# Kernel tuning notes

Measured on AMD Instinct MI355X. Metric: run time of the kernel, lower is better.

Reference implementation:

```python
import jax, jax.numpy as jnp
import numpy as np

N = 50000      # nodes
E = 600000     # edges
DIN = 128
H1, H2, H3 = 128, 128, 64
EPS = 1e-5


def setup_inputs() -> dict:
    key = jax.random.key(0)
    ks = jax.random.split(key, 12)
    x = jax.random.normal(ks[0], (N, DIN), jnp.float32)
    edge_index = jax.random.randint(ks[1], (2, E), 0, N, dtype=jnp.int32).astype(jnp.int64)
    s = lambda f: np.float32(1.0 / np.sqrt(f))
    W1 = jax.random.normal(ks[2], (DIN, H1), jnp.float32) * s(DIN)
    b1 = jnp.zeros((H1,), jnp.float32)
    W2 = jax.random.normal(ks[3], (H1, H2), jnp.float32) * s(H1)
    b2 = jnp.zeros((H2,), jnp.float32)
    W3 = jax.random.normal(ks[4], (H2, H3), jnp.float32) * s(H2)
    b3 = jnp.zeros((H3,), jnp.float32)
    g1 = 1.0 + 0.1 * jax.random.normal(ks[5], (H1,), jnp.float32)
    be1 = 0.1 * jax.random.normal(ks[6], (H1,), jnp.float32)
    g2 = 1.0 + 0.1 * jax.random.normal(ks[7], (H2,), jnp.float32)
    be2 = 0.1 * jax.random.normal(ks[8], (H2,), jnp.float32)
    return {"x": x, "edge_index": edge_index, "W1": W1, "b1": b1, "g1": g1,
            "be1": be1, "W2": W2, "b2": b2, "g2": g2, "be2": be2,
            "W3": W3, "b3": b3}


def _gcn(h_in, W, b, src_sl, dst_sl, norm, n):
    # GCNConv: h = X W; out_i = sum_{j->i} norm_ij * h_j + b  (self-loops included)
    h = h_in @ W
    msg = h[src_sl] * norm[:, None]          # [E+N, F] gather + scale
    out = jax.ops.segment_sum(msg, dst_sl, num_segments=n)
    return out + b


def _bn(x, g, b):
    # training-mode BatchNorm1d over nodes (biased variance, eps=1e-5)
    m = x.mean(0)
    v = x.var(0)
    return g * (x - m) * jax.lax.rsqrt(v + EPS) + b


def reference(x, edge_index, W1, b1, g1, be1, W2, b2, g2, be2, W3, b3):
    src, dst = edge_index[0], edge_index[1]
    loops = jnp.arange(N, dtype=src.dtype)
    src_sl = jnp.concatenate([src, loops])
    dst_sl = jnp.concatenate([dst, loops])
    deg = jax.ops.segment_sum(jnp.ones_like(dst_sl, jnp.float32), dst_sl,
                              num_segments=N)
    dinv = jnp.where(deg > 0, jax.lax.rsqrt(deg), 0.0)
    norm = dinv[src_sl] * dinv[dst_sl]       # symmetric D^-1/2 (A+I) D^-1/2

    h = _gcn(x, W1, b1, src_sl, dst_sl, norm, N)
    h = jax.nn.relu(_bn(h, g1, be1))         # dropout is identity in eval mode
    h = _gcn(h, W2, b2, src_sl, dst_sl, norm, N)
    h = jax.nn.relu(_bn(h, g2, be2))
    out = _gcn(h, W3, b3, src_sl, dst_sl, norm, N)  # [N, 64]
    return out
```

## Files before the change

### kernel.cpp

```cpp
#include <hip/hip_runtime.h>
#include <hip/hip_bf16.h>


typedef __attribute__((ext_vector_type(8))) short short8;
typedef __attribute__((ext_vector_type(4))) float f32x4;

__device__ inline unsigned short f2bf(float f) {
    unsigned int u = __float_as_uint(f);
    return (unsigned short)((u + 0x7fff + ((u >> 16) & 1)) >> 16);
}
__device__ inline float bf2f_lo(unsigned int p) { return __uint_as_float(p << 16); }
__device__ inline float bf2f_hi(unsigned int p) { return __uint_as_float(p & 0xffff0000u); }

__device__ inline void bf4_acc(uint2 v, float* a) {
    a[0] += bf2f_lo(v.x); a[1] += bf2f_hi(v.x);
    a[2] += bf2f_lo(v.y); a[3] += bf2f_hi(v.y);
}

__global__ void count_deg_kernel(const int* __restrict__ dst, int E,
                                 int* __restrict__ rowptr1) {
    int e = blockIdx.x * blockDim.x + threadIdx.x;
    if (e < E) atomicAdd(rowptr1 + dst[e], 1);
}

__global__ void dinv_deg_kernel(const int* __restrict__ rowptr, int n,
                                float* __restrict__ dinv, int* __restrict__ deg) {
    int i = blockIdx.x * blockDim.x + threadIdx.x;
    if (i < n) {
        int d = rowptr[i + 1];
        dinv[i] = rsqrtf((float)(d + 1));
        deg[i] = min(d, 63);
    }
}

__global__ void bhist_kernel(const int* __restrict__ deg, int n,
                             int* __restrict__ bh, int B) {
    __shared__ int lh[64];
    const int t = threadIdx.x;
    const int b = blockIdx.x;
    if (t < 64) lh[t] = 0;
    __syncthreads();
    const int lim = min((b + 1) * 2048, n);
    for (int i = b * 2048 + t; i < lim; i += 256) atomicAdd(&lh[deg[i]], 1);
    __syncthreads();
    if (t < 64) bh[t * B + b] = lh[t];
}

__global__ void bscan_kernel(int* __restrict__ bh, int total) {
    __shared__ int sh[256];
    const int t = threadIdx.x;
    int base = 0;
    for (int start = 0; start < total; start += 256) {
        int i = start + t;
        int v = (i < total) ? bh[i] : 0;
        sh[t] = v;
        __syncthreads();
#pragma unroll
        for (int off = 1; off < 256; off <<= 1) {
            int add = (t >= off) ? sh[t - off] : 0;
            __syncthreads();
            sh[t] += add;
            __syncthreads();
        }
        int excl = (t > 0 ? sh[t - 1] : 0) + base;
        if (i < total) bh[i] = excl;
        base += sh[255];
        __syncthreads();
    }
}

__global__ void place2_kernel(const int* __restrict__ deg, int n,
                              const int* __restrict__ bh, int B,
                              int* __restrict__ perm) {
    __shared__ int lbase[64];
    __shared__ int lcur[64];
    const int t = threadIdx.x;
    const int b = blockIdx.x;
    if (t < 64) {
        lbase[t] = bh[t * B + b];
        lcur[t] = 0;
    }
    __syncthreads();
    const int lim = min((b + 1) * 2048, n);
    for (int i = b * 2048 + t; i < lim; i += 256) {
        int d = deg[i];
        int r = atomicAdd(&lcur[d], 1);
        perm[lbase[d] + r] = i;
    }
}

__global__ __launch_bounds__(256) void scanA_kernel(int* __restrict__ data,
                                                    int total,
                                                    int* __restrict__ bsum) {
    __shared__ int sh[256];
    const int t = threadIdx.x;
    const int base = blockIdx.x * 2048 + t * 8;
    int v[8];
    int run = 0;
#pragma unroll
    for (int j = 0; j < 8; ++j) {
        int idx = base + j;
        int x = (idx < total) ? data[idx] : 0;
        run += x;
        v[j] = run;
    }
    sh[t] = run;
    __syncthreads();
#pragma unroll
    for (int off = 1; off < 256; off <<= 1) {
        int add = (t >= off) ? sh[t - off] : 0;
        __syncthreads();
        sh[t] += add;
        __syncthreads();
    }
    int prev = (t > 0) ? sh[t - 1] : 0;
#pragma unroll
    for (int j = 0; j < 8; ++j) {
        int idx = base + j;
        if (idx < total) data[idx] = v[j] + prev;
    }
    if (t == 255) bsum[blockIdx.x] = sh[255];
}

__global__ void scanB_kernel(int* __restrict__ bsum, int nb) {
    __shared__ int sh[64];
    const int t = threadIdx.x;
    sh[t] = (t < nb) ? bsum[t] : 0;
    __syncthreads();
#pragma unroll
    for (int off = 1; off < 64; off <<= 1) {
        int add = (t >= off) ? sh[t - off] : 0;
        __syncthreads();
        sh[t] += add;
        __syncthreads();
    }
    if (t < nb) bsum[t] = sh[t];
}

__global__ __launch_bounds__(256) void scanC_kernel(int* __restrict__ data,
                                                    int total,
                                                    const int* __restrict__ bsum) {
    if (blockIdx.x == 0) return;
    const int off = bsum[blockIdx.x - 1];
    const int base = blockIdx.x * 2048 + threadIdx.x * 8;
#pragma unroll
    for (int j = 0; j < 8; ++j) {
        int idx = base + j;
        if (idx < total) data[idx] += off;
    }
}

__global__ void csr_build_kernel(const int* __restrict__ src,
                                 const int* __restrict__ dst, int E,
                                 int* __restrict__ rowptr,
                                 int* __restrict__ csr_src) {
    int e = blockIdx.x * blockDim.x + threadIdx.x;
    if (e < E) {
        int pos = atomicAdd(rowptr + dst[e], 1);
        csr_src[pos] = src[e];
    }
}

__global__ void wt_bf16_kernel(const float* __restrict__ W, int NC,
                               unsigned short* __restrict__ Wt) {
    int idx = blockIdx.x * blockDim.x + threadIdx.x;
    if (idx < 128 * NC) {
        int k = idx / NC, nn = idx % NC;
        Wt[nn * 128 + k] = f2bf(W[idx]);
    }
}

__global__ void xcvt_kernel(const float* __restrict__ x,
                            unsigned short* __restrict__ xb, int total4) {
    int i = blockIdx.x * blockDim.x + threadIdx.x;
    if (i < total4) {
        float4 v = reinterpret_cast<const float4*>(x)[i];
        uint2 p;
        p.x = f2bf(v.x) | ((unsigned)f2bf(v.y) << 16);
        p.y = f2bf(v.z) | ((unsigned)f2bf(v.w) << 16);
        reinterpret_cast<uint2*>(xb)[i] = p;
    }
}

template <int NC, bool BN>
__global__ __launch_bounds__(256) void gemm_mfma(
    const unsigned short* __restrict__ A, const unsigned short* __restrict__ Wt,
    unsigned short* __restrict__ C, int n, const float* __restrict__ ss,
    const float* __restrict__ dinv) {
    __shared__ unsigned short Asd[64][136];
    __shared__ unsigned short Bsd[NC][136];
    const int tid = threadIdx.x;
    const int wave = tid >> 6;
    const int lane = tid & 63;
    const int row0 = blockIdx.x * 64;

    for (int idx = tid; idx < NC * 16; idx += 256) {
        int r = idx >> 4;
        int c = (idx & 15) * 8;
        uint4 v = *reinterpret_cast<const uint4*>(Wt + r * 128 + c);
        *reinterpret_cast<uint4*>(&Bsd[r][c]) = v;
    }
    for (int idx = tid; idx < 64 * 16; idx += 256) {
        int r = idx >> 4;
        int c = (idx & 15) * 8;
        int grow = row0 + r;
        uint4 v = make_uint4(0u, 0u, 0u, 0u);
        if (grow < n)
            v = *reinterpret_cast<const uint4*>(A + (size_t)grow * 128 + c);
        if (BN) {
            unsigned int p[4] = {v.x, v.y, v.z, v.w};
#pragma unroll
            for (int h = 0; h < 4; ++h) {
                int f = c + h * 2;
                float lo = fmaxf(fmaf(bf2f_lo(p[h]), ss[f], ss[128 + f]), 0.f);
                float hi = fmaxf(fmaf(bf2f_hi(p[h]), ss[f + 1], ss[129 + f]), 0.f);
                p[h] = f2bf(lo) | ((unsigned)f2bf(hi) << 16);
            }
            v = make_uint4(p[0], p[1], p[2], p[3]);
        }
        *reinterpret_cast<uint4*>(&Asd[r][c]) = v;
    }
    __syncthreads();

    f32x4 acc[NC / 16];
#pragma unroll
    for (int t = 0; t < NC / 16; ++t) acc[t] = (f32x4)(0.f);

    const int l15 = lane & 15;
    const int quad = lane >> 4;
#pragma unroll
    for (int kb = 0; kb < 128; kb += 32) {
        short8 a = *reinterpret_cast<const short8*>(&Asd[wave * 16 + l15][kb + quad * 8]);
#pragma unroll
        for (int t = 0; t < NC / 16; ++t) {
            short8 b = *reinterpret_cast<const short8*>(&Bsd[t * 16 + l15][kb + quad * 8]);
            acc[t] = __builtin_amdgcn_mfma_f32_16x16x32_bf16(a, b, acc[t], 0, 0, 0);
        }
    }

    const int rbase = row0 + wave * 16 + quad * 4;
    float dv[4] = {0.f, 0.f, 0.f, 0.f};
    if (rbase < n) {
        float4 d4 = *reinterpret_cast<const float4*>(dinv + rbase);
        dv[0] = d4.x; dv[1] = d4.y; dv[2] = d4.z; dv[3] = d4.w;
    }
#pragma unroll
    for (int t = 0; t < NC / 16; ++t) {
        int col = t * 16 + l15;
#pragma unroll
        for (int r = 0; r < 4; ++r) {
            int row = rbase + r;
            if (row < n)
                C[(size_t)row * NC + col] = f2bf(acc[t][r] * dv[r]);
        }
    }
}

template <int F, bool STATS, bool OBF>
__global__ __launch_bounds__(256) void aggregate_kernel(
    const unsigned short* __restrict__ hs, const int* __restrict__ csr_src,
    const int* __restrict__ rowptr, const int* __restrict__ perm,
    const float* __restrict__ dinv, const float* __restrict__ bias,
    void* __restrict__ outp, int n, float* __restrict__ stats) {
    const int LANES = F / 4;
    const int GROUPS = 256 / LANES;
    const int lane = threadIdx.x % LANES;
    const int grp = threadIdx.x / LANES;
    const int fq = lane * 4;
    const float4 b4 = *reinterpret_cast<const float4*>(bias + fq);
    float s[4] = {}, sq[4] = {};

    const int stride = gridDim.x * GROUPS * 4;

    for (int j0 = (blockIdx.x * GROUPS + grp) * 4; j0 < n; j0 += stride) {
        const int nv = min(4, n - j0);
        int nd[4], e[4], end[4];
        float acc[4][4] = {};
#pragma unroll
        for (int q = 0; q < 4; ++q) {
            if (q < nv) {
                int node = perm[j0 + q];
                nd[q] = node;
                e[q] = (node == 0) ? 0 : rowptr[node - 1];
                end[q] = rowptr[node];
            } else {
                nd[q] = -1; e[q] = 0; end[q] = 0;
            }
        }
#pragma unroll
        for (int q = 0; q < 4; ++q)
            if (nd[q] >= 0)
                bf4_acc(*reinterpret_cast<const uint2*>(hs + (size_t)nd[q] * F + fq), acc[q]);
        int rem = end[0] - e[0];
#pragma unroll
        for (int q = 1; q < 4; ++q)
            if (q < nv) rem = min(rem, end[q] - e[q]);
        for (; rem >= 2; rem -= 2) {
            int i0[4], i1[4];
#pragma unroll
            for (int q = 0; q < 4; ++q) {
                i0[q] = csr_src[e[q]];
                i1[q] = csr_src[e[q] + 1];
                e[q] += 2;
            }
            uint2 v0[4], v1[4];
#pragma unroll
            for (int q = 0; q < 4; ++q) {
                v0[q] = *reinterpret_cast<const uint2*>(hs + (size_t)i0[q] * F + fq);
                v1[q] = *reinterpret_cast<const uint2*>(hs + (size_t)i1[q] * F + fq);
            }
#pragma unroll
            for (int q = 0; q < 4; ++q) {
                bf4_acc(v0[q], acc[q]);
                bf4_acc(v1[q], acc[q]);
            }
        }
#pragma unroll
        for (int q = 0; q < 4; ++q) {
            for (; e[q] < end[q]; ++e[q]) {
                int s0 = csr_src[e[q]];
                bf4_acc(*reinterpret_cast<const uint2*>(hs + (size_t)s0 * F + fq), acc[q]);
            }
        }
#pragma unroll
        for (int q = 0; q < 4; ++q) {
            if (nd[q] < 0) continue;
            const float di = dinv[nd[q]];
            float y[4];
            y[0] = fmaf(di, acc[q][0], b4.x);
            y[1] = fmaf(di, acc[q][1], b4.y);
            y[2] = fmaf(di, acc[q][2], b4.z);
            y[3] = fmaf(di, acc[q][3], b4.w);
            if (OBF) {
                uint2 p;
                p.x = f2bf(y[0]) | ((unsigned)f2bf(y[1]) << 16);
                p.y = f2bf(y[2]) | ((unsigned)f2bf(y[3]) << 16);
                *reinterpret_cast<uint2*>((unsigned short*)outp + (size_t)nd[q] * F + fq) = p;
            } else {
                *reinterpret_cast<float4*>((float*)outp + (size_t)nd[q] * F + fq) =
                    make_float4(y[0], y[1], y[2], y[3]);
            }
            if (STATS) {
#pragma unroll
                for (int j = 0; j < 4; ++j) {
                    s[j] += y[j];
                    sq[j] = fmaf(y[j], y[j], sq[j]);
                }
            }
        }
    }

    if (STATS) {
        __shared__ float sred[32][8];
#pragma unroll
        for (int q = 0; q < 8; ++q) {
            float v = (q < 4) ? s[q] : sq[q - 4];
            sred[lane][grp] = v;
            __syncthreads();
            if (grp == 0) {
                float t = 0.f;
#pragma unroll
                for (int g = 0; g < 8; ++g) t += sred[lane][g];
                int f = fq + (q & 3);
                atomicAdd(stats + ((q < 4) ? f : 128 + f), t);
            }
            __syncthreads();
        }
    }
}

__global__ void finalize_kernel(const float* __restrict__ stats,
                                const float* __restrict__ g,
                                const float* __restrict__ be, float invn,
                                float* __restrict__ ss) {
    int f = threadIdx.x;
    float mean = stats[f] * invn;
    float var = fmaf(-mean, mean, stats[128 + f] * invn);
    float sc = g[f] * rsqrtf(var + 1e-5f);
    ss[f] = sc;
    ss[128 + f] = fmaf(-mean, sc, be[f]);
}

extern "C" void kernel_launch(void* const* d_in, const int* in_sizes, int n_in,
                              void* d_out, int out_size, void* d_ws,
                              size_t ws_size, hipStream_t stream) {
    const float* x   = (const float*)d_in[0];
    const int*   ei  = (const int*)d_in[1];
    const float* W1  = (const float*)d_in[2];
    const float* b1  = (const float*)d_in[3];
    const float* g1  = (const float*)d_in[4];
    const float* be1 = (const float*)d_in[5];
    const float* W2  = (const float*)d_in[6];
    const float* b2  = (const float*)d_in[7];
    const float* g2  = (const float*)d_in[8];
    const float* be2 = (const float*)d_in[9];
    const float* W3  = (const float*)d_in[10];
    const float* b3  = (const float*)d_in[11];
    float* out = (float*)d_out;

    const int n = in_sizes[0] / 128;
    const int E = in_sizes[1] / 2;
    const int* src = ei;
    const int* dst = ei + E;

    const int B = (n + 2047) / 2048;

    float* wsf    = (float*)d_ws;
    float* dinv   = wsf;
    float* stats  = dinv + n + 64;
    float* ss     = stats + 256;
    int*   rowptr = (int*)(ss + 256);
    int*   bsum   = rowptr + (n + 1);
    int*   bh     = bsum + 64;
    int*   deg    = bh + 64 * 32;
    int*   perm   = deg + n;
    int*   csrsrc = perm + n;
    unsigned short* wt1 = (unsigned short*)(csrsrc + E);
    unsigned short* wt2 = wt1 + 128 * 128;
    unsigned short* wt3 = wt2 + 128 * 128;
    unsigned short* abuf = wt3 + 64 * 128;
    unsigned short* hsb  = abuf + (size_t)n * 128;

    const int total = n + 1;
    const int nb = (total + 2047) / 2048;

    hipMemsetAsync(rowptr, 0, (size_t)total * 4, stream);
    count_deg_kernel<<<(E + 255) / 256, 256, 0, stream>>>(dst, E, rowptr + 1);
    dinv_deg_kernel<<<(n + 255) / 256, 256, 0, stream>>>(rowptr, n, dinv, deg);
    bhist_kernel<<<B, 256, 0, stream>>>(deg, n, bh, B);
    bscan_kernel<<<1, 256, 0, stream>>>(bh, 64 * B);
    place2_kernel<<<B, 256, 0, stream>>>(deg, n, bh, B, perm);
    scanA_kernel<<<nb, 256, 0, stream>>>(rowptr, total, bsum);
    scanB_kernel<<<1, 64, 0, stream>>>(bsum, nb);
    scanC_kernel<<<nb, 256, 0, stream>>>(rowptr, total, bsum);
    csr_build_kernel<<<(E + 255) / 256, 256, 0, stream>>>(src, dst, E, rowptr, csrsrc);
    wt_bf16_kernel<<<(128 * 128 + 255) / 256, 256, 0, stream>>>(W1, 128, wt1);
    wt_bf16_kernel<<<(128 * 128 + 255) / 256, 256, 0, stream>>>(W2, 128, wt2);
    wt_bf16_kernel<<<(128 * 64 + 255) / 256, 256, 0, stream>>>(W3, 64, wt3);
    xcvt_kernel<<<((n * 32) + 255) / 256, 256, 0, stream>>>(x, abuf, n * 32);

    const int gemmGrid = (n + 63) / 64;
    const int aggGrid = 512;

    gemm_mfma<128, false><<<gemmGrid, 256, 0, stream>>>(abuf, wt1, hsb, n, nullptr, dinv);
    hipMemsetAsync(stats, 0, 256 * 4, stream);
    aggregate_kernel<128, true, true><<<aggGrid, 256, 0, stream>>>(hsb, csrsrc, rowptr, perm, dinv, b1, abuf, n, stats);
    finalize_kernel<<<1, 128, 0, stream>>>(stats, g1, be1, 1.0f / n, ss);

    gemm_mfma<128, true><<<gemmGrid, 256, 0, stream>>>(abuf, wt2, hsb, n, ss, dinv);
    hipMemsetAsync(stats, 0, 256 * 4, stream);
    aggregate_kernel<128, true, true><<<aggGrid, 256, 0, stream>>>(hsb, csrsrc, rowptr, perm, dinv, b2, abuf, n, stats);
    finalize_kernel<<<1, 128, 0, stream>>>(stats, g2, be2, 1.0f / n, ss);

    gemm_mfma<64, true><<<gemmGrid, 256, 0, stream>>>(abuf, wt3, hsb, n, ss, dinv);
    aggregate_kernel<64, false, false><<<aggGrid, 256, 0, stream>>>(hsb, csrsrc, rowptr, perm, dinv, b3, out, n, nullptr);
}
```

Measured before the change: 465.2 us.

## Merge preprocessing and BN-finalize kernels to cut launch count

Folds degree counting, x/W bf16 conversion into one multi-role prep kernel, combines the dinv/histogram/scanA work into a prescan kernel, merges bucket placement with scanC, and moves BatchNorm finalize into the GEMM prologue. A single memset now zeroes both stats buffers and the degree array. This targets per-launch overhead and serialization across roughly a dozen small kernels. In exchange, every GEMM block recomputes the BN scale/shift, and kernels that mix roles have branch-divergent blocks.

```diff
diff --git a/kernel.cpp b/kernel.cpp
--- a/kernel.cpp
+++ b/kernel.cpp
@@ -17,42 +17,97 @@
     a[2] += bf2f_lo(v.y); a[3] += bf2f_hi(v.y);
 }
 
-__global__ void count_deg_kernel(const int* __restrict__ dst, int E,
-                                 int* __restrict__ rowptr1) {
-    int e = blockIdx.x * blockDim.x + threadIdx.x;
-    if (e < E) atomicAdd(rowptr1 + dst[e], 1);
-}
-
-__global__ void dinv_deg_kernel(const int* __restrict__ rowptr, int n,
-                                float* __restrict__ dinv, int* __restrict__ deg) {
-    int i = blockIdx.x * blockDim.x + threadIdx.x;
-    if (i < n) {
-        int d = rowptr[i + 1];
-        dinv[i] = rsqrtf((float)(d + 1));
-        deg[i] = min(d, 63);
-    }
-}
-
-__global__ void bhist_kernel(const int* __restrict__ deg, int n,
-                             int* __restrict__ bh, int B) {
+__global__ void prep_kernel(const int* __restrict__ dst, int E,
+                            int* __restrict__ deg,
+                            const float* __restrict__ x,
+                            unsigned short* __restrict__ xb, int total4,
+                            const float* __restrict__ W1,
+                            const float* __restrict__ W2,
+                            const float* __restrict__ W3,
+                            unsigned short* __restrict__ wt1,
+                            unsigned short* __restrict__ wt2,
+                            unsigned short* __restrict__ wt3,
+                            int EB, int XB) {
+    const int b = blockIdx.x;
+    const int t = threadIdx.x;
+    if (b < EB) {
+        int e = b * 256 + t;
+        if (e < E) atomicAdd(deg + dst[e], 1);
+    } else if (b < EB + XB) {
+        int i = (b - EB) * 256 + t;
+        if (i < total4) {
+            float4 v = reinterpret_cast<const float4*>(x)[i];
+            uint2 p;
+            p.x = f2bf(v.x) | ((unsigned)f2bf(v.y) << 16);
+            p.y = f2bf(v.z) | ((unsigned)f2bf(v.w) << 16);
+            reinterpret_cast<uint2*>(xb)[i] = p;
+        }
+    } else if (b < EB + XB + 64) {
+        int idx = (b - EB - XB) * 256 + t;
+        int k = idx >> 7, nn = idx & 127;
+        wt1[nn * 128 + k] = f2bf(W1[idx]);
+    } else if (b < EB + XB + 128) {
+        int idx = (b - EB - XB - 64) * 256 + t;
+        int k = idx >> 7, nn = idx & 127;
+        wt2[nn * 128 + k] = f2bf(W2[idx]);
+    } else {
+        int idx = (b - EB - XB - 128) * 256 + t;
+        int k = idx >> 6, nn = idx & 63;
+        wt3[nn * 128 + k] = f2bf(W3[idx]);
+    }
+}
+
+__global__ __launch_bounds__(256) void prescan_kernel(
+    const int* __restrict__ deg, int n, int B, float* __restrict__ dinv,
+    int* __restrict__ bh, int* __restrict__ rowptr, int* __restrict__ bsum) {
     __shared__ int lh[64];
-    const int t = threadIdx.x;
-    const int b = blockIdx.x;
+    __shared__ int sh[256];
+    const int t = threadIdx.x, b = blockIdx.x;
     if (t < 64) lh[t] = 0;
     __syncthreads();
-    const int lim = min((b + 1) * 2048, n);
-    for (int i = b * 2048 + t; i < lim; i += 256) atomicAdd(&lh[deg[i]], 1);
+    const int base = b * 2048 + t * 8;
+    int v[8];
+    int run = 0;
+#pragma unroll
+    for (int j = 0; j < 8; ++j) {
+        int idx = base + j;
+        int d = 0;
+        if (idx < n) {
+            d = deg[idx];
+            dinv[idx] = rsqrtf((float)(d + 1));
+            atomicAdd(&lh[min(d, 63)], 1);
+        }
+        run += d;
+        v[j] = run;
+    }
+    sh[t] = run;
     __syncthreads();
+#pragma unroll
+    for (int off = 1; off < 256; off <<= 1) {
+        int add = (t >= off) ? sh[t - off] : 0;
+        __syncthreads();
+        sh[t] += add;
+        __syncthreads();
+    }
+    int prev = (t > 0) ? sh[t - 1] : 0;
+#pragma unroll
+    for (int j = 0; j < 8; ++j) {
+        int idx = base + j;
+        if (idx < n) rowptr[idx + 1] = v[j] + prev;
+    }
+    if (t == 255) bsum[b] = sh[255];
+    if (b == 0 && t == 0) rowptr[0] = 0;
     if (t < 64) bh[t * B + b] = lh[t];
 }
 
-__global__ void bscan_kernel(int* __restrict__ bh, int total) {
+__global__ void midscan_kernel(int* __restrict__ bh, int totalbh,
+                               int* __restrict__ bsum, int B) {
     __shared__ int sh[256];
     const int t = threadIdx.x;
     int base = 0;
-    for (int start = 0; start < total; start += 256) {
+    for (int start = 0; start < totalbh; start += 256) {
         int i = start + t;
-        int v = (i < total) ? bh[i] : 0;
+        int v = (i < totalbh) ? bh[i] : 0;
         sh[t] = v;
         __syncthreads();
 #pragma unroll
@@ -63,90 +118,50 @@
             __syncthreads();
         }
         int excl = (t > 0 ? sh[t - 1] : 0) + base;
-        if (i < total) bh[i] = excl;
+        if (i < totalbh) bh[i] = excl;
         base += sh[255];
         __syncthreads();
     }
-}
-
-__global__ void place2_kernel(const int* __restrict__ deg, int n,
-                              const int* __restrict__ bh, int B,
-                              int* __restrict__ perm) {
-    __shared__ int lbase[64];
-    __shared__ int lcur[64];
+    int v = (t < B) ? bsum[t] : 0;
+    sh[t] = v;
+    __syncthreads();
+#pragma unroll
+    for (int off = 1; off < 64; off <<= 1) {
+        int add = (t >= off && t < 64) ? sh[t - off] : 0;
+        __syncthreads();
+        if (t < 64) sh[t] += add;
+        __syncthreads();
+    }
+    if (t < B) bsum[t] = sh[t];
+}
+
+__global__ void place_scanC_kernel(const int* __restrict__ deg, int n, int B,
+                                   const int* __restrict__ bh,
+                                   const int* __restrict__ bsum,
+                                   int* __restrict__ perm,
+                                   int* __restrict__ rowptr) {
     const int t = threadIdx.x;
-    const int b = blockIdx.x;
-    if (t < 64) {
-        lbase[t] = bh[t * B + b];
-        lcur[t] = 0;
-    }
-    __syncthreads();
-    const int lim = min((b + 1) * 2048, n);
-    for (int i = b * 2048 + t; i < lim; i += 256) {
-        int d = deg[i];
-        int r = atomicAdd(&lcur[d], 1);
-        perm[lbase[d] + r] = i;
-    }
-}
-
-__global__ __launch_bounds__(256) void scanA_kernel(int* __restrict__ data,
-                                                    int total,
-                                                    int* __restrict__ bsum) {
-    __shared__ int sh[256];
-    const int t = threadIdx.x;
-    const int base = blockIdx.x * 2048 + t * 8;
-    int v[8];
-    int run = 0;
-#pragma unroll
-    for (int j = 0; j < 8; ++j) {
-        int idx = base + j;
-        int x = (idx < total) ? data[idx] : 0;
-        run += x;
-        v[j] = run;
-    }
-    sh[t] = run;
-    __syncthreads();
-#pragma unroll
-    for (int off = 1; off < 256; off <<= 1) {
-        int add = (t >= off) ? sh[t - off] : 0;
-        __syncthreads();
-        sh[t] += add;
-        __syncthreads();
-    }
-    int prev = (t > 0) ? sh[t - 1] : 0;
-#pragma unroll
-    for (int j = 0; j < 8; ++j) {
-        int idx = base + j;
-        if (idx < total) data[idx] = v[j] + prev;
-    }
-    if (t == 255) bsum[blockIdx.x] = sh[255];
-}
-
-__global__ void scanB_kernel(int* __restrict__ bsum, int nb) {
-    __shared__ int sh[64];
-    const int t = threadIdx.x;
-    sh[t] = (t < nb) ? bsum[t] : 0;
-    __syncthreads();
-#pragma unroll
-    for (int off = 1; off < 64; off <<= 1) {
-        int add = (t >= off) ? sh[t - off] : 0;
-        __syncthreads();
-        sh[t] += add;
-        __syncthreads();
-    }
-    if (t < nb) bsum[t] = sh[t];
-}
-
-__global__ __launch_bounds__(256) void scanC_kernel(int* __restrict__ data,
-                                                    int total,
-                                                    const int* __restrict__ bsum) {
-    if (blockIdx.x == 0) return;
-    const int off = bsum[blockIdx.x - 1];
-    const int base = blockIdx.x * 2048 + threadIdx.x * 8;
-#pragma unroll
-    for (int j = 0; j < 8; ++j) {
-        int idx = base + j;
-        if (idx < total) data[idx] += off;
+    if ((int)blockIdx.x < B) {
+        const int b = blockIdx.x;
+        __shared__ int lbase[64];
+        __shared__ int lcur[64];
+        if (t < 64) {
+            lbase[t] = bh[t * B + b];
+            lcur[t] = 0;
+        }
+        __syncthreads();
+        const int lim = min((b + 1) * 2048, n);
+        for (int i = b * 2048 + t; i < lim; i += 256) {
+            int d = min(deg[i], 63);
+            int r = atomicAdd(&lcur[d], 1);
+            perm[lbase[d] + r] = i;
+        }
+    } else {
+        const int c = blockIdx.x - B;
+        if (c == 0) return;
+        const int off = bsum[c - 1];
+        const int lim = min((c + 1) * 2048, n);
+        for (int i = c * 2048 + t; i < lim; i += 256) rowptr[i + 1] += off;
     }
 }
 
@@ -161,38 +176,30 @@
     }
 }
 
-__global__ void wt_bf16_kernel(const float* __restrict__ W, int NC,
-                               unsigned short* __restrict__ Wt) {
-    int idx = blockIdx.x * blockDim.x + threadIdx.x;
-    if (idx < 128 * NC) {
-        int k = idx / NC, nn = idx % NC;
-        Wt[nn * 128 + k] = f2bf(W[idx]);
-    }
-}
-
-__global__ void xcvt_kernel(const float* __restrict__ x,
-                            unsigned short* __restrict__ xb, int total4) {
-    int i = blockIdx.x * blockDim.x + threadIdx.x;
-    if (i < total4) {
-        float4 v = reinterpret_cast<const float4*>(x)[i];
-        uint2 p;
-        p.x = f2bf(v.x) | ((unsigned)f2bf(v.y) << 16);
-        p.y = f2bf(v.z) | ((unsigned)f2bf(v.w) << 16);
-        reinterpret_cast<uint2*>(xb)[i] = p;
-    }
-}
-
 template <int NC, bool BN>
 __global__ __launch_bounds__(256) void gemm_mfma(
     const unsigned short* __restrict__ A, const unsigned short* __restrict__ Wt,
-    unsigned short* __restrict__ C, int n, const float* __restrict__ ss,
+    unsigned short* __restrict__ C, int n, const float* __restrict__ stats,
+    const float* __restrict__ g, const float* __restrict__ be, float invn,
     const float* __restrict__ dinv) {
     __shared__ unsigned short Asd[64][136];
     __shared__ unsigned short Bsd[NC][136];
+    __shared__ float ssl[256];
     const int tid = threadIdx.x;
     const int wave = tid >> 6;
     const int lane = tid & 63;
     const int row0 = blockIdx.x * 64;
+
+    if (BN) {
+        if (tid < 128) {
+            float mean = stats[tid] * invn;
+            float var = fmaf(-mean, mean, stats[128 + tid] * invn);
+            float sc = g[tid] * rsqrtf(var + 1e-5f);
+            ssl[tid] = sc;
+            ssl[128 + tid] = fmaf(-mean, sc, be[tid]);
+        }
+        __syncthreads();
+    }
 
     for (int idx = tid; idx < NC * 16; idx += 256) {
         int r = idx >> 4;
@@ -212,8 +219,8 @@
 #pragma unroll
             for (int h = 0; h < 4; ++h) {
                 int f = c + h * 2;
-                float lo = fmaxf(fmaf(bf2f_lo(p[h]), ss[f], ss[128 + f]), 0.f);
-                float hi = fmaxf(fmaf(bf2f_hi(p[h]), ss[f + 1], ss[129 + f]), 0.f);
+                float lo = fmaxf(fmaf(bf2f_lo(p[h]), ssl[f], ssl[128 + f]), 0.f);
+                float hi = fmaxf(fmaf(bf2f_hi(p[h]), ssl[f + 1], ssl[129 + f]), 0.f);
                 p[h] = f2bf(lo) | ((unsigned)f2bf(hi) << 16);
             }
             v = make_uint4(p[0], p[1], p[2], p[3]);
@@ -369,18 +376,6 @@
     }
 }
 
-__global__ void finalize_kernel(const float* __restrict__ stats,
-                                const float* __restrict__ g,
-                                const float* __restrict__ be, float invn,
-                                float* __restrict__ ss) {
-    int f = threadIdx.x;
-    float mean = stats[f] * invn;
-    float var = fmaf(-mean, mean, stats[128 + f] * invn);
-    float sc = g[f] * rsqrtf(var + 1e-5f);
-    ss[f] = sc;
-    ss[128 + f] = fmaf(-mean, sc, be[f]);
-}
-
 extern "C" void kernel_launch(void* const* d_in, const int* in_sizes, int n_in,
                               void* d_out, int out_size, void* d_ws,
                               size_t ws_size, hipStream_t stream) {
@@ -406,14 +401,14 @@
     const int B = (n + 2047) / 2048;
 
     float* wsf    = (float*)d_ws;
-    float* dinv   = wsf;
-    float* stats  = dinv + n + 64;
-    float* ss     = stats + 256;
-    int*   rowptr = (int*)(ss + 256);
-    int*   bsum   = rowptr + (n + 1);
-    int*   bh     = bsum + 64;
-    int*   deg    = bh + 64 * 32;
-    int*   perm   = deg + n;
+    float* stats1 = wsf;
+    float* stats2 = stats1 + 256;
+    int*   deg    = (int*)(stats2 + 256);
+    float* dinv   = (float*)(deg + n);
+    int*   bh     = (int*)(dinv + n + 64);
+    int*   bsum   = bh + 64 * 32;
+    int*   rowptr = bsum + 64;
+    int*   perm   = rowptr + (n + 1);
     int*   csrsrc = perm + n;
     unsigned short* wt1 = (unsigned short*)(csrsrc + E);
     unsigned short* wt2 = wt1 + 128 * 128;
@@ -421,37 +416,27 @@
     unsigned short* abuf = wt3 + 64 * 128;
     unsigned short* hsb  = abuf + (size_t)n * 128;
 
-    const int total = n + 1;
-    const int nb = (total + 2047) / 2048;
-
-    hipMemsetAsync(rowptr, 0, (size_t)total * 4, stream);
-    count_deg_kernel<<<(E + 255) / 256, 256, 0, stream>>>(dst, E, rowptr + 1);
-    dinv_deg_kernel<<<(n + 255) / 256, 256, 0, stream>>>(rowptr, n, dinv, deg);
-    bhist_kernel<<<B, 256, 0, stream>>>(deg, n, bh, B);
-    bscan_kernel<<<1, 256, 0, stream>>>(bh, 64 * B);
-    place2_kernel<<<B, 256, 0, stream>>>(deg, n, bh, B, perm);
-    scanA_kernel<<<nb, 256, 0, stream>>>(rowptr, total, bsum);
-    scanB_kernel<<<1, 64, 0, stream>>>(bsum, nb);
-    scanC_kernel<<<nb, 256, 0, stream>>>(rowptr, total, bsum);
-    csr_build_kernel<<<(E + 255) / 256, 256, 0, stream>>>(src, dst, E, rowptr, csrsrc);
-    wt_bf16_kernel<<<(128 * 128 + 255) / 256, 256, 0, stream>>>(W1, 128, wt1);
-    wt_bf16_kernel<<<(128 * 128 + 255) / 256, 256, 0, stream>>>(W2, 128, wt2);
-    wt_bf16_kernel<<<(128 * 64 + 255) / 256, 256, 0, stream>>>(W3, 64, wt3);
-    xcvt_kernel<<<((n * 32) + 255) / 256, 256, 0, stream>>>(x, abuf, n * 32);
+    const int EB = (E + 255) / 256;
+    const int total4 = n * 32;
+    const int XB = (total4 + 255) / 256;
+
+    hipMemsetAsync(wsf, 0, (size_t)(512 + n) * 4, stream);
+    prep_kernel<<<EB + XB + 160, 256, 0, stream>>>(dst, E, deg, x, abuf, total4,
+                                                   W1, W2, W3, wt1, wt2, wt3,
+                                                   EB, XB);
+    prescan_kernel<<<B, 256, 0, stream>>>(deg, n, B, dinv, bh, rowptr, bsum);
+    midscan_kernel<<<1, 256, 0, stream>>>(bh, 64 * B, bsum, B);
+    place_scanC_kernel<<<2 * B, 256, 0, stream>>>(deg, n, B, bh, bsum, perm, rowptr);
+    csr_build_kernel<<<EB, 256, 0, stream>>>(src, dst, E, rowptr, csrsrc);
 
     const int gemmGrid = (n + 63) / 64;
     const int aggGrid = 512;
-
-    gemm_mfma<128, false><<<gemmGrid, 256, 0, stream>>>(abuf, wt1, hsb, n, nullptr, dinv);
-    hipMemsetAsync(stats, 0, 256 * 4, stream);
-    aggregate_kernel<128, true, true><<<aggGrid, 256, 0, stream>>>(hsb, csrsrc, rowptr, perm, dinv, b1, abuf, n, stats);
-    finalize_kernel<<<1, 128, 0, stream>>>(stats, g1, be1, 1.0f / n, ss);
-
-    gemm_mfma<128, true><<<gemmGrid, 256, 0, stream>>>(abuf, wt2, hsb, n, ss, dinv);
-    hipMemsetAsync(stats, 0, 256 * 4, stream);
-    aggregate_kernel<128, true, true><<<aggGrid, 256, 0, stream>>>(hsb, csrsrc, rowptr, perm, dinv, b2, abuf, n, stats);
-    finalize_kernel<<<1, 128, 0, stream>>>(stats, g2, be2, 1.0f / n, ss);
-
-    gemm_mfma<64, true><<<gemmGrid, 256, 0, stream>>>(abuf, wt3, hsb, n, ss, dinv);
+    const float invn = 1.0f / n;
+
+    gemm_mfma<128, false><<<gemmGrid, 256, 0, stream>>>(abuf, wt1, hsb, n, nullptr, nullptr, nullptr, invn, dinv);
+    aggregate_kernel<128, true, true><<<aggGrid, 256, 0, stream>>>(hsb, csrsrc, rowptr, perm, dinv, b1, abuf, n, stats1);
+    gemm_mfma<128, true><<<gemmGrid, 256, 0, stream>>>(abuf, wt2, hsb, n, stats1, g1, be1, invn, dinv);
+    aggregate_kernel<128, true, true><<<aggGrid, 256, 0, stream>>>(hsb, csrsrc, rowptr, perm, dinv, b2, abuf, n, stats2);
+    gemm_mfma<64, true><<<gemmGrid, 256, 0, stream>>>(abuf, wt3, hsb, n, stats2, g2, be2, invn, dinv);
     aggregate_kernel<64, false, false><<<aggGrid, 256, 0, stream>>>(hsb, csrsrc, rowptr, perm, dinv, b3, out, n, nullptr);
 }
```

Result: faster. 436.9 us (-6.1%).
